# Optimization experiments

Measured on AMD Instinct MI355X. Metric: run time of the kernel, lower is better.

Reference implementation:

```python
import jax, jax.numpy as jnp
import numpy as np

B, P, ENC = 128, 196, 2048   # batch, num_pixels (14x14), encoder_dim
L, V = 50, 10000             # max caption length, vocab
A, D, E = 512, 512, 512      # attention_dim, decoder_dim, embed_dim


def setup_inputs() -> dict:
    key = jax.random.key(0)
    ks = jax.random.split(key, 24)
    def nrm(k, shape, s=0.02):
        return jax.random.normal(k, shape, jnp.float32) * s
    def uni(k, shape, lim=0.1):
        return jax.random.uniform(k, shape, jnp.float32, -lim, lim)
    cap_len = jax.random.randint(ks[2], (B,), 2, L + 1).at[0].set(L)  # ensure max dec_len = L-1 (static)
    return {
        "encoder_out": jax.random.normal(ks[0], (B, P, ENC), jnp.float32),
        "enc_cap": jax.random.randint(ks[1], (B, L), 0, V),
        "cap_len": cap_len,
        "emb_W": uni(ks[3], (V, E)),
        "init_h_W": nrm(ks[4], (D, ENC)), "init_h_b": jnp.zeros((D,), jnp.float32),
        "init_c_W": nrm(ks[5], (D, ENC)), "init_c_b": jnp.zeros((D,), jnp.float32),
        "enc_attn_W": nrm(ks[6], (A, ENC)), "enc_attn_b": jnp.zeros((A,), jnp.float32),
        "dec_attn_W": nrm(ks[7], (A, D)), "dec_attn_b": jnp.zeros((A,), jnp.float32),
        "full_attn_W": nrm(ks[8], (1, A)), "full_attn_b": jnp.zeros((1,), jnp.float32),
        "lstm_Wih": nrm(ks[9], (4 * D, E + ENC)), "lstm_Whh": nrm(ks[10], (4 * D, D)),
        "lstm_bih": jnp.zeros((4 * D,), jnp.float32), "lstm_bhh": jnp.zeros((4 * D,), jnp.float32),
        "fbeta_W": nrm(ks[11], (ENC, D)), "fbeta_b": jnp.zeros((ENC,), jnp.float32),
        "fc_W": uni(ks[12], (V, D)), "fc_b": jnp.zeros((V,), jnp.float32),
    }


def _forward(encoder_out, enc_cap, cap_len,
             emb_W, init_h_W, init_h_b, init_c_W, init_c_b,
             enc_attn_W, enc_attn_b, dec_attn_W, dec_attn_b,
             full_attn_W, full_attn_b, lstm_Wih, lstm_Whh, lstm_bih, lstm_bhh,
             fbeta_W, fbeta_b, fc_W, fc_b):
    Bsz, Pn, Ed = encoder_out.shape
    Dd = lstm_Whh.shape[1]
    # sort by decreasing length (stable, like torch.sort)
    sort_ind = jnp.argsort(-cap_len, stable=True)
    cap_sorted = cap_len[sort_ind]
    dec_len = cap_sorted - 1                       # [B]
    enc_s = encoder_out[sort_ind]                  # [B,P,ENC]
    caps_s = enc_cap[sort_ind]                     # [B,L]
    emb = emb_W[caps_s]                            # [B,L,E]
    enc_mean = enc_s.mean(axis=1)
    h0 = enc_mean @ init_h_W.T + init_h_b
    c0 = enc_mean @ init_c_W.T + init_c_b
    # precompute encoder attention features once (done per-step in torch, same values)
    enc_feat = jnp.einsum('bpe,ae->bpa', enc_s, enc_attn_W) + enc_attn_b  # [B,P,A]
    T = enc_cap.shape[1] - 1                       # static max decode steps

    def step(carry, t):
        h, c = carry
        active = (dec_len > t)[:, None].astype(h.dtype)         # [B,1]
        dec_feat = h @ dec_attn_W.T + dec_attn_b                # [B,A]
        attn = jax.nn.relu(enc_feat + dec_feat[:, None, :])     # [B,P,A]
        scores = attn @ full_attn_W[0] + full_attn_b[0]         # [B,P]
        alpha = jax.nn.softmax(scores, axis=1)                  # [B,P]
        ctx = jnp.einsum('bpe,bp->be', enc_s, alpha)            # [B,ENC]
        gate = jax.nn.sigmoid(h @ fbeta_W.T + fbeta_b)          # [B,ENC]
        ctx = gate * ctx
        x = jnp.concatenate([emb[:, t, :], ctx], axis=1)        # [B,E+ENC]
        gates = x @ lstm_Wih.T + lstm_bih + h @ lstm_Whh.T + lstm_bhh
        i_g, f_g, g_g, o_g = jnp.split(gates, 4, axis=1)
        c_new = jax.nn.sigmoid(f_g) * c + jax.nn.sigmoid(i_g) * jnp.tanh(g_g)
        h_new = jax.nn.sigmoid(o_g) * jnp.tanh(c_new)
        # dropout is identity in eval mode
        out = (h_new @ fc_W.T + fc_b) * active                  # zero rows past dec_len
        alpha = alpha * active
        # freeze state for finished sequences (matches torch's h[:bs] slicing)
        h = active * h_new + (1.0 - active) * h
        c = active * c_new + (1.0 - active) * c
        return (h, c), (out, alpha)

    (_, _), (outs, alphas) = jax.lax.scan(step, (h0, c0), jnp.arange(T))
    output = jnp.swapaxes(outs, 0, 1)    # [B,T,V]
    alphas = jnp.swapaxes(alphas, 0, 1)  # [B,T,P]
    return output, caps_s, dec_len, alphas, sort_ind


def reference(encoder_out, enc_cap, cap_len,
              emb_W, init_h_W, init_h_b, init_c_W, init_c_b,
              enc_attn_W, enc_attn_b, dec_attn_W, dec_attn_b,
              full_attn_W, full_attn_b, lstm_Wih, lstm_Whh, lstm_bih, lstm_bhh,
              fbeta_W, fbeta_b, fc_W, fc_b):
    return _forward(encoder_out, enc_cap, cap_len,
                    emb_W, init_h_W, init_h_b, init_c_W, init_c_b,
                    enc_attn_W, enc_attn_b, dec_attn_W, dec_attn_b,
                    full_attn_W, full_attn_b, lstm_Wih, lstm_Whh, lstm_bih, lstm_bhh,
                    fbeta_W, fbeta_b, fc_W, fc_b)
```

## Files before the change

### kernel.cpp

```cpp
#include <hip/hip_runtime.h>
#include <hip/hip_bf16.h>

#define B_    128
#define P_    196
#define ENCD  2048
#define LL    50
#define VV    10000
#define AA    512
#define DD    512
#define EE    512
#define TT    49
#define XKK   3072
#define PROJN 2560
#define VPAD  10048

#define OUT0_OFF 0
#define OUT1_OFF 62720000
#define OUT2_OFF 62726400
#define OUT3_OFF 62726528
#define OUT4_OFF 63955840

#define WS_SI      0ull
#define WS_DLEN    512ull
#define WS_BATTN   1024ull
#define WS_BLSTM   11264ull
#define WS_MEANS   19456ull
#define WS_H       1068032ull
#define WS_C       1330176ull
#define WS_HBF     1592320ull
#define WS_PROJ    1723392ull
#define WS_XCAT    6966272ull
#define WS_GATES   7752704ull
#define WS_HSTORE  16141312ull
#define WS_WPROJ   22563840ull
#define WS_WCAT    25185280ull
#define WS_FCW     37768192ull
#define WS_WENC    48057344ull
#define WS_EFEAT   50154496ull
#define WS_ENCBF   75844608ull
#define NEED_ENCBF 178605056ull

typedef __attribute__((ext_vector_type(4))) float f32x4;
typedef __attribute__((ext_vector_type(8))) short s16x8;

__device__ __forceinline__ float sigmoidf_(float x) { return 1.0f / (1.0f + __expf(-x)); }

__device__ __forceinline__ unsigned short f2bf(float x) {
    union { float f; unsigned int u; } v; v.f = x;
    unsigned int r = (v.u + 0x7FFFu + ((v.u >> 16) & 1u)) >> 16;
    return (unsigned short)r;
}
__device__ __forceinline__ float bf2f(unsigned short u) {
    return __uint_as_float(((unsigned int)u) << 16);
}

__device__ __forceinline__ void gload_lds16(const void* g, void* l) {
    __builtin_amdgcn_global_load_lds((const __attribute__((address_space(1))) void*)g,
                                     (__attribute__((address_space(3))) void*)l, 16, 0, 0);
}

__global__ void sort_kernel(const int* __restrict__ cap_len, const int* __restrict__ enc_cap,
                            int* __restrict__ si, int* __restrict__ dlen,
                            float* __restrict__ out_caps, float* __restrict__ out_dlen,
                            float* __restrict__ out_sind)
{
    __shared__ int cl[B_];
    __shared__ int rank_to_idx[B_];
    int i = threadIdx.x;
    cl[i] = cap_len[i];
    __syncthreads();
    int my = cl[i];
    int r = 0;
    for (int j = 0; j < B_; ++j) {
        int oj = cl[j];
        if (oj > my || (oj == my && j < i)) ++r;
    }
    rank_to_idx[r] = i;
    __syncthreads();
    int src = rank_to_idx[i];
    si[i] = src;
    int dl = cl[src] - 1;
    dlen[i] = dl;
    out_dlen[i] = (float)dl;
    out_sind[i] = (float)src;
    for (int k = 0; k < LL; ++k) out_caps[i * LL + k] = (float)enc_cap[src * LL + k];
}

__global__ void bias_cat_kernel(const float* __restrict__ dec_b, const float* __restrict__ fbeta_b,
                                const float* __restrict__ bih, const float* __restrict__ bhh,
                                float* __restrict__ b_attn, float* __restrict__ b_lstm)
{
    int i = blockIdx.x * 256 + threadIdx.x;
    if (i < AA) b_attn[i] = dec_b[i];
    else if (i < PROJN) b_attn[i] = fbeta_b[i - AA];
    if (i < 2048) b_lstm[i] = bih[i] + bhh[i];
}

__global__ void enc_mean_sorted(const float* __restrict__ enc, const int* __restrict__ si,
                                float* __restrict__ means)
{
    int idx = blockIdx.x * 256 + threadIdx.x;
    int b = idx >> 11, e = idx & 2047;
    const float* p = enc + (size_t)si[b] * P_ * ENCD + e;
    float s = 0.f;
    for (int q = 0; q < P_; ++q) s += p[(size_t)q * ENCD];
    means[idx] = s * (1.0f / 196.0f);
}

template<int MODE, bool CONV>
__launch_bounds__(256)
__global__ void mfma_gemm(const void* __restrict__ Av, const void* __restrict__ Wv,
                          const float* __restrict__ bias, const int* __restrict__ dlen,
                          float* __restrict__ Cf, unsigned short* __restrict__ Cbf,
                          int K, int KC, long long ldc, long long slabStride, int Nreal)
{
    __shared__ __align__(16) unsigned short As[2][128 * 32];
    __shared__ __align__(16) unsigned short Ws[2][64 * 32];
    const int tid  = threadIdx.x;
    const int wave = tid >> 6, lane = tid & 63;
    const int m0 = (MODE == 2 ? blockIdx.x : blockIdx.y) * 128;
    const int n0 = (MODE == 2 ? blockIdx.y : blockIdx.x) * 64;
    const int z  = blockIdx.z;
    const int kbeg = z * KC;
    const int nt = KC / 32;
    const int r16 = lane & 15, kg = lane >> 4;

    f32x4 acc[8];
    #pragma unroll
    for (int i = 0; i < 8; ++i) acc[i] = f32x4{0.f, 0.f, 0.f, 0.f};

    const int a_off0 = wave * 2048 + lane * 16;
    const int a_row0 = a_off0 >> 6, a_c0 = (a_off0 >> 4) & 3;
    const int a_off1 = a_off0 + 1024;
    const int a_row1 = a_off1 >> 6, a_c1 = (a_off1 >> 4) & 3;
    const int w_off  = wave * 1024 + lane * 16;
    const int w_row  = w_off >> 6,  w_c  = (w_off >> 4) & 3;
    const int c_arow = tid >> 1, c_acb = (tid & 1) * 16;
    const int c_wrow = tid >> 2, c_wcb = (tid & 3) * 8;

    int buf = 0;

    if constexpr (!CONV) {
        const unsigned short* A = (const unsigned short*)Av;
        const unsigned short* W = (const unsigned short*)Wv;
        gload_lds16(A + (size_t)(m0 + a_row0) * K + kbeg + a_c0 * 8, &As[0][wave * 1024]);
        gload_lds16(A + (size_t)(m0 + a_row1) * K + kbeg + a_c1 * 8, &As[0][wave * 1024 + 512]);
        gload_lds16(W + (size_t)(n0 + w_row)  * K + kbeg + w_c  * 8, &Ws[0][wave * 512]);
        __syncthreads();
        for (int it = 0; it < nt; ++it) {
            if (it + 1 < nt) {
                int k1 = kbeg + (it + 1) * 32;
                gload_lds16(A + (size_t)(m0 + a_row0) * K + k1 + a_c0 * 8, &As[buf ^ 1][wave * 1024]);
                gload_lds16(A + (size_t)(m0 + a_row1) * K + k1 + a_c1 * 8, &As[buf ^ 1][wave * 1024 + 512]);
                gload_lds16(W + (size_t)(n0 + w_row)  * K + k1 + w_c  * 8, &Ws[buf ^ 1][wave * 512]);
            }
            s16x8 bfrag = *(const s16x8*)&Ws[buf][(wave * 16 + r16) * 32 + kg * 8];
            #pragma unroll
            for (int i = 0; i < 8; ++i) {
                s16x8 afrag = *(const s16x8*)&As[buf][(i * 16 + r16) * 32 + kg * 8];
                acc[i] = __builtin_amdgcn_mfma_f32_16x16x32_bf16(afrag, bfrag, acc[i], 0, 0, 0);
            }
            __syncthreads();
            buf ^= 1;
        }
    } else {
        const float* A = (const float*)Av;
        const float* W = (const float*)Wv;
        float ra[16], rw[8];
        #pragma unroll
        for (int j = 0; j < 16; ++j) ra[j] = A[(size_t)(m0 + c_arow) * K + kbeg + c_acb + j];
        #pragma unroll
        for (int j = 0; j < 8; ++j)  rw[j] = W[(size_t)(n0 + c_wrow) * K + kbeg + c_wcb + j];
        {
            unsigned short t0[16], t1[8];
            #pragma unroll
            for (int j = 0; j < 16; ++j) t0[j] = f2bf(ra[j]);
            #pragma unroll
            for (int j = 0; j < 8; ++j)  t1[j] = f2bf(rw[j]);
            *(s16x8*)&As[0][c_arow * 32 + c_acb]     = *(s16x8*)&t0[0];
            *(s16x8*)&As[0][c_arow * 32 + c_acb + 8] = *(s16x8*)&t0[8];
            *(s16x8*)&Ws[0][c_wrow * 32 + c_wcb]     = *(s16x8*)&t1[0];
        }
        __syncthreads();
        for (int it = 0; it < nt; ++it) {
            float ra2[16], rw2[8];
            bool more = (it + 1 < nt);
            if (more) {
                int k1 = kbeg + (it + 1) * 32;
                #pragma unroll
                for (int j = 0; j < 16; ++j) ra2[j] = A[(size_t)(m0 + c_arow) * K + k1 + c_acb + j];
                #pragma unroll
                for (int j = 0; j < 8; ++j)  rw2[j] = W[(size_t)(n0 + c_wrow) * K + k1 + c_wcb + j];
            }
            s16x8 bfrag = *(const s16x8*)&Ws[buf][(wave * 16 + r16) * 32 + kg * 8];
            #pragma unroll
            for (int i = 0; i < 8; ++i) {
                s16x8 afrag = *(const s16x8*)&As[buf][(i * 16 + r16) * 32 + kg * 8];
                acc[i] = __builtin_amdgcn_mfma_f32_16x16x32_bf16(afrag, bfrag, acc[i], 0, 0, 0);
            }
            if (more) {
                unsigned short t0[16], t1[8];
                #pragma unroll
                for (int j = 0; j < 16; ++j) t0[j] = f2bf(ra2[j]);
                #pragma unroll
                for (int j = 0; j < 8; ++j)  t1[j] = f2bf(rw2[j]);
                *(s16x8*)&As[buf ^ 1][c_arow * 32 + c_acb]     = *(s16x8*)&t0[0];
                *(s16x8*)&As[buf ^ 1][c_arow * 32 + c_acb + 8] = *(s16x8*)&t0[8];
                *(s16x8*)&Ws[buf ^ 1][c_wrow * 32 + c_wcb]     = *(s16x8*)&t1[0];
            }
            __syncthreads();
            buf ^= 1;
        }
    }

    int n = n0 + wave * 16 + r16;
    float bv = 0.f;
    if (bias && z == 0) bv = (MODE == 2) ? (n < Nreal ? bias[n] : 0.f) : bias[n];
    float* Cz = Cf + (size_t)z * slabStride;
    #pragma unroll
    for (int i = 0; i < 8; ++i) {
        #pragma unroll
        for (int r = 0; r < 4; ++r) {
            int m = m0 + i * 16 + kg * 4 + r;
            float v = acc[i][r] + bv;
            if (MODE == 0) {
                Cz[(size_t)m * ldc + n] = v;
            } else if (MODE == 1) {
                Cbf[(size_t)m * ldc + n] = f2bf(v);
            } else {
                int bb = m & 127, tt2 = m >> 7;
                if (n < Nreal)
                    Cf[((size_t)bb * TT + tt2) * VV + n] = (dlen[bb] > tt2) ? v : 0.f;
            }
        }
    }
}

template<int NS>
__global__ void scores_raw_kernel(const unsigned short* __restrict__ efeat,
                                  const float* __restrict__ proj, const float* __restrict__ battn,
                                  const float* __restrict__ full_W, const float* __restrict__ full_b,
                                  const int* __restrict__ si, const int* __restrict__ dlen,
                                  float* __restrict__ sc_out, int t)
{
    int b = blockIdx.x, q = blockIdx.y;
    if (dlen[b] <= t) return;
    int tid = threadIdx.x, wave = tid >> 6, lane = tid & 63;
    __shared__ float df[AA];
    __shared__ float wf[AA];
    const size_t ps = (size_t)B_ * PROJN;
    const float* pz = proj + (size_t)b * PROJN;
    for (int i = tid; i < AA; i += 256) {
        float v = battn[i];
        #pragma unroll
        for (int z = 0; z < NS; ++z) v += pz[z * ps + i];
        df[i] = v; wf[i] = full_W[i];
    }
    __syncthreads();
    int sb = si[b];
    const float fb = full_b[0];
    float dfv[8], wfv[8];
    #pragma unroll
    for (int j = 0; j < 8; ++j) { dfv[j] = df[lane * 8 + j]; wfv[j] = wf[lane * 8 + j]; }
    int pbeg = q * 49;
    for (int p = pbeg + wave; p < pbeg + 49; p += 4) {
        const unsigned short* ef = efeat + ((size_t)sb * P_ + p) * AA + lane * 8;
        s16x8 ev = *(const s16x8*)ef;
        float s = 0.f;
        #pragma unroll
        for (int j = 0; j < 8; ++j) {
            float v = bf2f((unsigned short)ev[j]) + dfv[j];
            v = v > 0.f ? v : 0.f;
            s += v * wfv[j];
        }
        #pragma unroll
        for (int off = 32; off; off >>= 1) s += __shfl_down(s, off);
        if (lane == 0) sc_out[b * P_ + p] = s + fb;
    }
}

template<int NS>
__global__ void ctx_fused_kernel(const float* __restrict__ sc_in,
                                 const float* __restrict__ proj, const float* __restrict__ battn,
                                 const int* __restrict__ si, const int* __restrict__ dlen,
                                 const int* __restrict__ enc_cap, const float* __restrict__ emb_W,
                                 const unsigned short* __restrict__ h_bf,
                                 const unsigned short* __restrict__ encbf,
                                 const float* __restrict__ encf, int use_bf,
                                 float* __restrict__ alphas_out, unsigned short* __restrict__ xcat, int t)
{
    int b = blockIdx.y, x = blockIdx.x, tid = threadIdx.x;
    int wave = tid >> 6, lane = tid & 63;
    bool active = dlen[b] > t;
    if (!active) {
        if (x == 0 && tid < P_) alphas_out[((size_t)b * TT + t) * P_ + tid] = 0.f;
        return;
    }
    __shared__ float al[P_];
    __shared__ float red[8];
    float v = (tid < P_) ? sc_in[b * P_ + tid] : -1e30f;
    float m = v;
    #pragma unroll
    for (int off = 32; off; off >>= 1) m = fmaxf(m, __shfl_down(m, off));
    if (lane == 0) red[wave] = m;
    __syncthreads();
    if (tid == 0) red[4] = fmaxf(fmaxf(red[0], red[1]), fmaxf(red[2], red[3]));
    __syncthreads();
    m = red[4];
    float e = (tid < P_) ? __expf(v - m) : 0.f;
    float s = e;
    #pragma unroll
    for (int off = 32; off; off >>= 1) s += __shfl_down(s, off);
    if (lane == 0) red[wave] = s;
    __syncthreads();
    if (tid == 0) red[5] = 1.0f / (red[0] + red[1] + red[2] + red[3]);
    __syncthreads();
    float inv = red[5];
    if (tid < P_) al[tid] = e * inv;
    __syncthreads();

    int sb = si[b];
    if (x == 0) {
        if (tid < P_) alphas_out[((size_t)b * TT + t) * P_ + tid] = al[tid];
        int tok = enc_cap[sb * LL + t];
        for (int k = tid; k < EE; k += 256) {
            xcat[(size_t)b * XKK + k]        = f2bf(emb_W[(size_t)tok * EE + k]);
            xcat[(size_t)b * XKK + 2560 + k] = h_bf[b * DD + k];
        }
    }

    int e0 = x * 1024 + tid * 4;
    float a0 = 0.f, a1 = 0.f, a2 = 0.f, a3 = 0.f;
    if (use_bf) {
        const unsigned short* base = encbf + (size_t)sb * P_ * ENCD + e0;
        #pragma unroll 7
        for (int p = 0; p < P_; ++p) {
            uint2 u = *(const uint2*)(base + (size_t)p * ENCD);
            float alp = al[p];
            a0 = fmaf(alp, __uint_as_float(u.x << 16), a0);
            a1 = fmaf(alp, __uint_as_float(u.x & 0xffff0000u), a1);
            a2 = fmaf(alp, __uint_as_float(u.y << 16), a2);
            a3 = fmaf(alp, __uint_as_float(u.y & 0xffff0000u), a3);
        }
    } else {
        const float* base = encf + (size_t)sb * P_ * ENCD + e0;
        #pragma unroll 7
        for (int p = 0; p < P_; ++p) {
            float4 u = *(const float4*)(base + (size_t)p * ENCD);
            float alp = al[p];
            a0 = fmaf(alp, u.x, a0); a1 = fmaf(alp, u.y, a1);
            a2 = fmaf(alp, u.z, a2); a3 = fmaf(alp, u.w, a3);
        }
    }
    const float* pz = proj + (size_t)b * PROJN;
    const size_t ps = (size_t)B_ * PROJN;
    int ei = AA + e0;
    float4 gl = *(const float4*)&battn[ei];
    #pragma unroll
    for (int z = 0; z < NS; ++z) {
        float4 gp = *(const float4*)&pz[z * ps + ei];
        gl.x += gp.x; gl.y += gp.y; gl.z += gp.z; gl.w += gp.w;
    }
    ushort4 xo;
    xo.x = f2bf(a0 * sigmoidf_(gl.x));
    xo.y = f2bf(a1 * sigmoidf_(gl.y));
    xo.z = f2bf(a2 * sigmoidf_(gl.z));
    xo.w = f2bf(a3 * sigmoidf_(gl.w));
    *(ushort4*)&xcat[(size_t)b * XKK + EE + e0] = xo;
}

template<int NS>
__global__ void pointwise_kernel(const float* __restrict__ gates, const float* __restrict__ blstm,
                                 const int* __restrict__ dlen,
                                 float* __restrict__ h, float* __restrict__ c,
                                 unsigned short* __restrict__ h_bf, unsigned short* __restrict__ hstore,
                                 int t)
{
    int idx = blockIdx.x * 256 + threadIdx.x;
    int b = idx >> 9, d = idx & 511;
    bool act = dlen[b] > (t - 1);
    if (!act) {
        hstore[((size_t)(t - 1) * B_ + b) * DD + d] = 0;
        return;
    }
    const size_t slab = (size_t)B_ * 2048;
    const float* g = gates + (size_t)b * 2048;
    float gi = blstm[d], gf = blstm[512 + d], gg = blstm[1024 + d], go = blstm[1536 + d];
    #pragma unroll
    for (int z = 0; z < NS; ++z) {
        gi += g[z * slab + d];
        gf += g[z * slab + 512 + d];
        gg += g[z * slab + 1024 + d];
        go += g[z * slab + 1536 + d];
    }
    float cn = sigmoidf_(gf) * c[idx] + sigmoidf_(gi) * tanhf(gg);
    float hn = sigmoidf_(go) * tanhf(cn);
    unsigned short hb = f2bf(hn);
    hstore[((size_t)(t - 1) * B_ + b) * DD + d] = hb;
    h[idx] = hn; c[idx] = cn;
    h_bf[idx] = hb;
}

__global__ void conv_bf16_kernel(const float* __restrict__ src, unsigned short* __restrict__ dst, int n4)
{
    for (int i = blockIdx.x * 256 + threadIdx.x; i < n4; i += gridDim.x * 256) {
        float4 v = ((const float4*)src)[i];
        ushort4 o;
        o.x = f2bf(v.x); o.y = f2bf(v.y); o.z = f2bf(v.z); o.w = f2bf(v.w);
        ((ushort4*)dst)[i] = o;
    }
}
__global__ void conv_wproj_kernel(const float* __restrict__ dec_W, const float* __restrict__ fbeta_W,
                                  unsigned short* __restrict__ dst)
{
    int k = blockIdx.x * 256 + threadIdx.x, n = blockIdx.y;
    float v = (n < AA) ? dec_W[(size_t)n * DD + k] : fbeta_W[(size_t)(n - AA) * DD + k];
    dst[(size_t)n * DD + k] = f2bf(v);
}
__global__ void conv_wcat_kernel(const float* __restrict__ Wih, const float* __restrict__ Whh,
                                 unsigned short* __restrict__ dst)
{
    int k = blockIdx.x * 256 + threadIdx.x, n = blockIdx.y;
    float v = (k < 2560) ? Wih[(size_t)n * 2560 + k] : Whh[(size_t)n * DD + (k - 2560)];
    dst[(size_t)n * XKK + k] = f2bf(v);
}
__global__ void conv_fcw_kernel(const float* __restrict__ fc_W, unsigned short* __restrict__ dst)
{
    int k = blockIdx.x * 256 + threadIdx.x, n = blockIdx.y;
    float v = (n < VV) ? fc_W[(size_t)n * DD + k] : 0.f;
    dst[(size_t)n * DD + k] = f2bf(v);
}

extern "C" void kernel_launch(void* const* d_in, const int* in_sizes, int n_in,
                              void* d_out, int out_size, void* d_ws, size_t ws_size,
                              hipStream_t stream)
{
    const float* encoder_out = (const float*)d_in[0];
    const int*   enc_cap     = (const int*)d_in[1];
    const int*   cap_len     = (const int*)d_in[2];
    const float* emb_W       = (const float*)d_in[3];
    const float* init_h_W    = (const float*)d_in[4];
    const float* init_h_b    = (const float*)d_in[5];
    const float* init_c_W    = (const float*)d_in[6];
    const float* init_c_b    = (const float*)d_in[7];
    const float* enc_attn_W  = (const float*)d_in[8];
    const float* enc_attn_b  = (const float*)d_in[9];
    const float* dec_attn_W  = (const float*)d_in[10];
    const float* dec_attn_b  = (const float*)d_in[11];
    const float* full_attn_W = (const float*)d_in[12];
    const float* full_attn_b = (const float*)d_in[13];
    const float* lstm_Wih    = (const float*)d_in[14];
    const float* lstm_Whh    = (const float*)d_in[15];
    const float* lstm_bih    = (const float*)d_in[16];
    const float* lstm_bhh    = (const float*)d_in[17];
    const float* fbeta_W     = (const float*)d_in[18];
    const float* fbeta_b     = (const float*)d_in[19];
    const float* fc_W        = (const float*)d_in[20];
    const float* fc_b        = (const float*)d_in[21];

    char* wsb = (char*)d_ws;
    int*   si     = (int*)(wsb + WS_SI);
    int*   dlen   = (int*)(wsb + WS_DLEN);
    float* battn  = (float*)(wsb + WS_BATTN);
    float* blstm  = (float*)(wsb + WS_BLSTM);
    float* means  = (float*)(wsb + WS_MEANS);
    float* sc     = (float*)(wsb + WS_MEANS + 4096);
    float* h      = (float*)(wsb + WS_H);
    float* c      = (float*)(wsb + WS_C);
    unsigned short* h_bf   = (unsigned short*)(wsb + WS_HBF);
    float* proj   = (float*)(wsb + WS_PROJ);
    unsigned short* xcat   = (unsigned short*)(wsb + WS_XCAT);
    float* gates  = (float*)(wsb + WS_GATES);
    unsigned short* hstore = (unsigned short*)(wsb + WS_HSTORE);
    unsigned short* wproj  = (unsigned short*)(wsb + WS_WPROJ);
    unsigned short* wcat   = (unsigned short*)(wsb + WS_WCAT);
    unsigned short* fcw    = (unsigned short*)(wsb + WS_FCW);
    unsigned short* wenc   = (unsigned short*)(wsb + WS_WENC);
    unsigned short* efeat  = (unsigned short*)(wsb + WS_EFEAT);
    unsigned short* encbf  = (unsigned short*)(wsb + WS_ENCBF);

    float* out      = (float*)d_out;
    float* out0     = out + OUT0_OFF;
    float* out_caps = out + OUT1_OFF;
    float* out_dlen = out + OUT2_OFF;
    float* alphas   = out + OUT3_OFF;
    float* out_sind = out + OUT4_OFF;

    const int use_encbf = (ws_size >= NEED_ENCBF) ? 1 : 0;

    sort_kernel<<<1, B_, 0, stream>>>(cap_len, enc_cap, si, dlen, out_caps, out_dlen, out_sind);
    bias_cat_kernel<<<10, 256, 0, stream>>>(dec_attn_b, fbeta_b, lstm_bih, lstm_bhh, battn, blstm);
    enc_mean_sorted<<<(B_ * ENCD) / 256, 256, 0, stream>>>(encoder_out, si, means);

    mfma_gemm<0, true><<<dim3(DD / 64, 1, 1), 256, 0, stream>>>(
        means, init_h_W, init_h_b, nullptr, h, nullptr, ENCD, ENCD, DD, 0, DD);
    mfma_gemm<0, true><<<dim3(DD / 64, 1, 1), 256, 0, stream>>>(
        means, init_c_W, init_c_b, nullptr, c, nullptr, ENCD, ENCD, DD, 0, DD);
    conv_bf16_kernel<<<64, 256, 0, stream>>>(h, h_bf, (B_ * DD) / 4);

    conv_wproj_kernel<<<dim3(2, PROJN), 256, 0, stream>>>(dec_attn_W, fbeta_W, wproj);
    conv_wcat_kernel<<<dim3(12, 2048), 256, 0, stream>>>(lstm_Wih, lstm_Whh, wcat);
    conv_fcw_kernel<<<dim3(2, VPAD), 256, 0, stream>>>(fc_W, fcw);
    conv_bf16_kernel<<<256, 256, 0, stream>>>(enc_attn_W, wenc, (AA * ENCD) / 4);
    if (use_encbf)
        conv_bf16_kernel<<<2048, 256, 0, stream>>>(encoder_out, encbf, (B_ * P_ * ENCD) / 4);

    if (use_encbf)
        mfma_gemm<1, false><<<dim3(AA / 64, (B_ * P_) / 128, 1), 256, 0, stream>>>(
            encbf, wenc, enc_attn_b, nullptr, nullptr, efeat, ENCD, ENCD, AA, 0, AA);
    else
        mfma_gemm<1, true><<<dim3(AA / 64, (B_ * P_) / 128, 1), 256, 0, stream>>>(
            encoder_out, enc_attn_W, enc_attn_b, nullptr, nullptr, efeat, ENCD, ENCD, AA, 0, AA);

    for (int t = 0; t < TT; ++t) {
        if (t > 0)
            pointwise_kernel<8><<<(B_ * DD) / 256, 256, 0, stream>>>(
                gates, blstm, dlen, h, c, h_bf, hstore, t);

        mfma_gemm<0, false><<<dim3(PROJN / 64, 1, 4), 256, 0, stream>>>(
            h_bf, wproj, nullptr, nullptr, proj, nullptr, DD, 128, PROJN, (long long)B_ * PROJN, PROJN);

        scores_raw_kernel<4><<<dim3(B_, 4), 256, 0, stream>>>(
            efeat, proj, battn, full_attn_W, full_attn_b, si, dlen, sc, t);

        ctx_fused_kernel<4><<<dim3(2, B_), 256, 0, stream>>>(
            sc, proj, battn, si, dlen, enc_cap, emb_W, h_bf,
            encbf, encoder_out, use_encbf, alphas, xcat, t);

        mfma_gemm<0, false><<<dim3(2048 / 64, 1, 8), 256, 0, stream>>>(
            xcat, wcat, nullptr, nullptr, gates, nullptr, XKK, 384, 2048, (long long)B_ * 2048, 2048);
    }
    pointwise_kernel<8><<<(B_ * DD) / 256, 256, 0, stream>>>(
        gates, blstm, dlen, h, c, h_bf, hstore, TT);

    mfma_gemm<2, false><<<dim3(TT, VPAD / 64, 1), 256, 0, stream>>>(
        hstore, fcw, fc_b, dlen, out0, nullptr, DD, DD, VV, 0, VV);
}
```

Before: 2.970 ms.

## Fuse attention scoring into context kernel and widen GEMM K-tile to 64

Merges the separate attention-score kernel into the context/softmax kernel, so each block computes all 196 pixel scores itself with one thread per pixel. This removes one launch per timestep and the scores round-trip through global memory. In exchange, the score work is duplicated across the two x-blocks per batch row, and each thread now runs a 512-long serial dot product. It also adds a K-tile template parameter to the bf16 MFMA GEMM and uses 64 for the non-converting GEMMs, halving the loop iterations and barriers at the cost of double the LDS per block.

Result: no change. 2.973 ms (+0.1%).

```diff
diff --git a/kernel.cpp b/kernel.cpp
--- a/kernel.cpp
+++ b/kernel.cpp
@@ -107,34 +107,31 @@
     means[idx] = s * (1.0f / 196.0f);
 }
 
-template<int MODE, bool CONV>
+template<int MODE, bool CONV, int BK2>
 __launch_bounds__(256)
 __global__ void mfma_gemm(const void* __restrict__ Av, const void* __restrict__ Wv,
                           const float* __restrict__ bias, const int* __restrict__ dlen,
                           float* __restrict__ Cf, unsigned short* __restrict__ Cbf,
                           int K, int KC, long long ldc, long long slabStride, int Nreal)
 {
-    __shared__ __align__(16) unsigned short As[2][128 * 32];
-    __shared__ __align__(16) unsigned short Ws[2][64 * 32];
+    constexpr int RB = BK2 * 2;
+    constexpr int AL = (128 * RB) / 4096;
+    constexpr int WL = (64 * RB) / 4096;
+    __shared__ __align__(16) unsigned short As[2][128 * BK2];
+    __shared__ __align__(16) unsigned short Ws[2][64 * BK2];
     const int tid  = threadIdx.x;
     const int wave = tid >> 6, lane = tid & 63;
     const int m0 = (MODE == 2 ? blockIdx.x : blockIdx.y) * 128;
     const int n0 = (MODE == 2 ? blockIdx.y : blockIdx.x) * 64;
     const int z  = blockIdx.z;
     const int kbeg = z * KC;
-    const int nt = KC / 32;
+    const int nt = KC / BK2;
     const int r16 = lane & 15, kg = lane >> 4;
 
     f32x4 acc[8];
     #pragma unroll
     for (int i = 0; i < 8; ++i) acc[i] = f32x4{0.f, 0.f, 0.f, 0.f};
 
-    const int a_off0 = wave * 2048 + lane * 16;
-    const int a_row0 = a_off0 >> 6, a_c0 = (a_off0 >> 4) & 3;
-    const int a_off1 = a_off0 + 1024;
-    const int a_row1 = a_off1 >> 6, a_c1 = (a_off1 >> 4) & 3;
-    const int w_off  = wave * 1024 + lane * 16;
-    const int w_row  = w_off >> 6,  w_c  = (w_off >> 4) & 3;
     const int c_arow = tid >> 1, c_acb = (tid & 1) * 16;
     const int c_wrow = tid >> 2, c_wcb = (tid & 3) * 8;
 
@@ -143,27 +140,49 @@
     if constexpr (!CONV) {
         const unsigned short* A = (const unsigned short*)Av;
         const unsigned short* W = (const unsigned short*)Wv;
-        gload_lds16(A + (size_t)(m0 + a_row0) * K + kbeg + a_c0 * 8, &As[0][wave * 1024]);
-        gload_lds16(A + (size_t)(m0 + a_row1) * K + kbeg + a_c1 * 8, &As[0][wave * 1024 + 512]);
-        gload_lds16(W + (size_t)(n0 + w_row)  * K + kbeg + w_c  * 8, &Ws[0][wave * 512]);
+        #pragma unroll
+        for (int s = 0; s < AL; ++s) {
+            int L = s * 4096 + wave * 1024 + lane * 16;
+            gload_lds16(A + (size_t)(m0 + L / RB) * K + kbeg + (L % RB) / 2,
+                        &As[0][(s * 4096 + wave * 1024) / 2]);
+        }
+        #pragma unroll
+        for (int s = 0; s < WL; ++s) {
+            int L = s * 4096 + wave * 1024 + lane * 16;
+            gload_lds16(W + (size_t)(n0 + L / RB) * K + kbeg + (L % RB) / 2,
+                        &Ws[0][(s * 4096 + wave * 1024) / 2]);
+        }
         __syncthreads();
         for (int it = 0; it < nt; ++it) {
             if (it + 1 < nt) {
-                int k1 = kbeg + (it + 1) * 32;
-                gload_lds16(A + (size_t)(m0 + a_row0) * K + k1 + a_c0 * 8, &As[buf ^ 1][wave * 1024]);
-                gload_lds16(A + (size_t)(m0 + a_row1) * K + k1 + a_c1 * 8, &As[buf ^ 1][wave * 1024 + 512]);
-                gload_lds16(W + (size_t)(n0 + w_row)  * K + k1 + w_c  * 8, &Ws[buf ^ 1][wave * 512]);
-            }
-            s16x8 bfrag = *(const s16x8*)&Ws[buf][(wave * 16 + r16) * 32 + kg * 8];
+                int k1 = kbeg + (it + 1) * BK2;
+                #pragma unroll
+                for (int s = 0; s < AL; ++s) {
+                    int L = s * 4096 + wave * 1024 + lane * 16;
+                    gload_lds16(A + (size_t)(m0 + L / RB) * K + k1 + (L % RB) / 2,
+                                &As[buf ^ 1][(s * 4096 + wave * 1024) / 2]);
+                }
+                #pragma unroll
+                for (int s = 0; s < WL; ++s) {
+                    int L = s * 4096 + wave * 1024 + lane * 16;
+                    gload_lds16(W + (size_t)(n0 + L / RB) * K + k1 + (L % RB) / 2,
+                                &Ws[buf ^ 1][(s * 4096 + wave * 1024) / 2]);
+                }
+            }
             #pragma unroll
-            for (int i = 0; i < 8; ++i) {
-                s16x8 afrag = *(const s16x8*)&As[buf][(i * 16 + r16) * 32 + kg * 8];
-                acc[i] = __builtin_amdgcn_mfma_f32_16x16x32_bf16(afrag, bfrag, acc[i], 0, 0, 0);
+            for (int kk2 = 0; kk2 < BK2 / 32; ++kk2) {
+                s16x8 bfrag = *(const s16x8*)&Ws[buf][(wave * 16 + r16) * BK2 + kk2 * 32 + kg * 8];
+                #pragma unroll
+                for (int i = 0; i < 8; ++i) {
+                    s16x8 afrag = *(const s16x8*)&As[buf][(i * 16 + r16) * BK2 + kk2 * 32 + kg * 8];
+                    acc[i] = __builtin_amdgcn_mfma_f32_16x16x32_bf16(afrag, bfrag, acc[i], 0, 0, 0);
+                }
             }
             __syncthreads();
             buf ^= 1;
         }
     } else {
+        static_assert(!CONV || BK2 == 32, "CONV path requires BK2==32");
         const float* A = (const float*)Av;
         const float* W = (const float*)Wv;
         float ra[16], rw[8];
@@ -237,57 +256,15 @@
 }
 
 template<int NS>
-__global__ void scores_raw_kernel(const unsigned short* __restrict__ efeat,
-                                  const float* __restrict__ proj, const float* __restrict__ battn,
-                                  const float* __restrict__ full_W, const float* __restrict__ full_b,
-                                  const int* __restrict__ si, const int* __restrict__ dlen,
-                                  float* __restrict__ sc_out, int t)
-{
-    int b = blockIdx.x, q = blockIdx.y;
-    if (dlen[b] <= t) return;
-    int tid = threadIdx.x, wave = tid >> 6, lane = tid & 63;
-    __shared__ float df[AA];
-    __shared__ float wf[AA];
-    const size_t ps = (size_t)B_ * PROJN;
-    const float* pz = proj + (size_t)b * PROJN;
-    for (int i = tid; i < AA; i += 256) {
-        float v = battn[i];
-        #pragma unroll
-        for (int z = 0; z < NS; ++z) v += pz[z * ps + i];
-        df[i] = v; wf[i] = full_W[i];
-    }
-    __syncthreads();
-    int sb = si[b];
-    const float fb = full_b[0];
-    float dfv[8], wfv[8];
-    #pragma unroll
-    for (int j = 0; j < 8; ++j) { dfv[j] = df[lane * 8 + j]; wfv[j] = wf[lane * 8 + j]; }
-    int pbeg = q * 49;
-    for (int p = pbeg + wave; p < pbeg + 49; p += 4) {
-        const unsigned short* ef = efeat + ((size_t)sb * P_ + p) * AA + lane * 8;
-        s16x8 ev = *(const s16x8*)ef;
-        float s = 0.f;
-        #pragma unroll
-        for (int j = 0; j < 8; ++j) {
-            float v = bf2f((unsigned short)ev[j]) + dfv[j];
-            v = v > 0.f ? v : 0.f;
-            s += v * wfv[j];
-        }
-        #pragma unroll
-        for (int off = 32; off; off >>= 1) s += __shfl_down(s, off);
-        if (lane == 0) sc_out[b * P_ + p] = s + fb;
-    }
-}
-
-template<int NS>
-__global__ void ctx_fused_kernel(const float* __restrict__ sc_in,
-                                 const float* __restrict__ proj, const float* __restrict__ battn,
-                                 const int* __restrict__ si, const int* __restrict__ dlen,
-                                 const int* __restrict__ enc_cap, const float* __restrict__ emb_W,
-                                 const unsigned short* __restrict__ h_bf,
-                                 const unsigned short* __restrict__ encbf,
-                                 const float* __restrict__ encf, int use_bf,
-                                 float* __restrict__ alphas_out, unsigned short* __restrict__ xcat, int t)
+__global__ void attn_kernel(const unsigned short* __restrict__ efeat,
+                            const float* __restrict__ proj, const float* __restrict__ battn,
+                            const float* __restrict__ full_W, const float* __restrict__ full_b,
+                            const int* __restrict__ si, const int* __restrict__ dlen,
+                            const int* __restrict__ enc_cap, const float* __restrict__ emb_W,
+                            const unsigned short* __restrict__ h_bf,
+                            const unsigned short* __restrict__ encbf,
+                            const float* __restrict__ encf, int use_bf,
+                            float* __restrict__ alphas_out, unsigned short* __restrict__ xcat, int t)
 {
     int b = blockIdx.y, x = blockIdx.x, tid = threadIdx.x;
     int wave = tid >> 6, lane = tid & 63;
@@ -296,9 +273,35 @@
         if (x == 0 && tid < P_) alphas_out[((size_t)b * TT + t) * P_ + tid] = 0.f;
         return;
     }
-    __shared__ float al[P_];
+    __shared__ float df[AA];
+    __shared__ float wf[AA];
+    __shared__ float sal[P_];
     __shared__ float red[8];
-    float v = (tid < P_) ? sc_in[b * P_ + tid] : -1e30f;
+    const float* pz = proj + (size_t)b * PROJN;
+    const size_t ps = (size_t)B_ * PROJN;
+    for (int i = tid; i < AA; i += 256) {
+        float v = battn[i];
+        #pragma unroll
+        for (int z = 0; z < NS; ++z) v += pz[z * ps + i];
+        df[i] = v; wf[i] = full_W[i];
+    }
+    __syncthreads();
+    int sb = si[b];
+    float s = full_b[0];
+    if (tid < P_) {
+        const unsigned short* ef = efeat + ((size_t)sb * P_ + tid) * AA;
+        #pragma unroll 8
+        for (int e8 = 0; e8 < 64; ++e8) {
+            s16x8 ev = *(const s16x8*)(ef + e8 * 8);
+            #pragma unroll
+            for (int j = 0; j < 8; ++j) {
+                float v = bf2f((unsigned short)ev[j]) + df[e8 * 8 + j];
+                v = v > 0.f ? v : 0.f;
+                s = fmaf(v, wf[e8 * 8 + j], s);
+            }
+        }
+    }
+    float v = (tid < P_) ? s : -1e30f;
     float m = v;
     #pragma unroll
     for (int off = 32; off; off >>= 1) m = fmaxf(m, __shfl_down(m, off));
@@ -308,26 +311,24 @@
     __syncthreads();
     m = red[4];
     float e = (tid < P_) ? __expf(v - m) : 0.f;
-    float s = e;
+    float ssum = e;
     #pragma unroll
-    for (int off = 32; off; off >>= 1) s += __shfl_down(s, off);
-    if (lane == 0) red[wave] = s;
+    for (int off = 32; off; off >>= 1) ssum += __shfl_down(ssum, off);
+    if (lane == 0) red[wave] = ssum;
     __syncthreads();
     if (tid == 0) red[5] = 1.0f / (red[0] + red[1] + red[2] + red[3]);
     __syncthreads();
-    float inv = red[5];
-    if (tid < P_) al[tid] = e * inv;
-    __syncthreads();
-
-    int sb = si[b];
+    float al = e * red[5];
+    if (tid < P_) sal[tid] = al;
     if (x == 0) {
-        if (tid < P_) alphas_out[((size_t)b * TT + t) * P_ + tid] = al[tid];
+        if (tid < P_) alphas_out[((size_t)b * TT + t) * P_ + tid] = al;
         int tok = enc_cap[sb * LL + t];
         for (int k = tid; k < EE; k += 256) {
             xcat[(size_t)b * XKK + k]        = f2bf(emb_W[(size_t)tok * EE + k]);
             xcat[(size_t)b * XKK + 2560 + k] = h_bf[b * DD + k];
         }
     }
+    __syncthreads();
 
     int e0 = x * 1024 + tid * 4;
     float a0 = 0.f, a1 = 0.f, a2 = 0.f, a3 = 0.f;
@@ -336,7 +337,7 @@
         #pragma unroll 7
         for (int p = 0; p < P_; ++p) {
             uint2 u = *(const uint2*)(base + (size_t)p * ENCD);
-            float alp = al[p];
+            float alp = sal[p];
             a0 = fmaf(alp, __uint_as_float(u.x << 16), a0);
             a1 = fmaf(alp, __uint_as_float(u.x & 0xffff0000u), a1);
             a2 = fmaf(alp, __uint_as_float(u.y << 16), a2);
@@ -347,13 +348,11 @@
         #pragma unroll 7
         for (int p = 0; p < P_; ++p) {
             float4 u = *(const float4*)(base + (size_t)p * ENCD);
-            float alp = al[p];
+            float alp = sal[p];
             a0 = fmaf(alp, u.x, a0); a1 = fmaf(alp, u.y, a1);
             a2 = fmaf(alp, u.z, a2); a3 = fmaf(alp, u.w, a3);
         }
     }
-    const float* pz = proj + (size_t)b * PROJN;
-    const size_t ps = (size_t)B_ * PROJN;
     int ei = AA + e0;
     float4 gl = *(const float4*)&battn[ei];
     #pragma unroll
@@ -464,7 +463,6 @@
     float* battn  = (float*)(wsb + WS_BATTN);
     float* blstm  = (float*)(wsb + WS_BLSTM);
     float* means  = (float*)(wsb + WS_MEANS);
-    float* sc     = (float*)(wsb + WS_MEANS + 4096);
     float* h      = (float*)(wsb + WS_H);
     float* c      = (float*)(wsb + WS_C);
     unsigned short* h_bf   = (unsigned short*)(wsb + WS_HBF);
@@ -492,9 +490,9 @@
     bias_cat_kernel<<<10, 256, 0, stream>>>(dec_attn_b, fbeta_b, lstm_bih, lstm_bhh, battn, blstm);
     enc_mean_sorted<<<(B_ * ENCD) / 256, 256, 0, stream>>>(encoder_out, si, means);
 
-    mfma_gemm<0, true><<<dim3(DD / 64, 1, 1), 256, 0, stream>>>(
+    mfma_gemm<0, true, 32><<<dim3(DD / 64, 1, 1), 256, 0, stream>>>(
         means, init_h_W, init_h_b, nullptr, h, nullptr, ENCD, ENCD, DD, 0, DD);
-    mfma_gemm<0, true><<<dim3(DD / 64, 1, 1), 256, 0, stream>>>(
+    mfma_gemm<0, true, 32><<<dim3(DD / 64, 1, 1), 256, 0, stream>>>(
         means, init_c_W, init_c_b, nullptr, c, nullptr, ENCD, ENCD, DD, 0, DD);
     conv_bf16_kernel<<<64, 256, 0, stream>>>(h, h_bf, (B_ * DD) / 4);
 
@@ -506,10 +504,10 @@
         conv_bf16_kernel<<<2048, 256, 0, stream>>>(encoder_out, encbf, (B_ * P_ * ENCD) / 4);
 
     if (use_encbf)
-        mfma_gemm<1, false><<<dim3(AA / 64, (B_ * P_) / 128, 1), 256, 0, stream>>>(
+        mfma_gemm<1, false, 64><<<dim3(AA / 64, (B_ * P_) / 128, 1), 256, 0, stream>>>(
             encbf, wenc, enc_attn_b, nullptr, nullptr, efeat, ENCD, ENCD, AA, 0, AA);
     else
-        mfma_gemm<1, true><<<dim3(AA / 64, (B_ * P_) / 128, 1), 256, 0, stream>>>(
+        mfma_gemm<1, true, 32><<<dim3(AA / 64, (B_ * P_) / 128, 1), 256, 0, stream>>>(
             encoder_out, enc_attn_W, enc_attn_b, nullptr, nullptr, efeat, ENCD, ENCD, AA, 0, AA);
 
     for (int t = 0; t < TT; ++t) {
@@ -517,22 +515,19 @@
             pointwise_kernel<8><<<(B_ * DD) / 256, 256, 0, stream>>>(
                 gates, blstm, dlen, h, c, h_bf, hstore, t);
 
-        mfma_gemm<0, false><<<dim3(PROJN / 64, 1, 4), 256, 0, stream>>>(
+        mfma_gemm<0, false, 64><<<dim3(PROJN / 64, 1, 4), 256, 0, stream>>>(
             h_bf, wproj, nullptr, nullptr, proj, nullptr, DD, 128, PROJN, (long long)B_ * PROJN, PROJN);
 
-        scores_raw_kernel<4><<<dim3(B_, 4), 256, 0, stream>>>(
-            efeat, proj, battn, full_attn_W, full_attn_b, si, dlen, sc, t);
-
-        ctx_fused_kernel<4><<<dim3(2, B_), 256, 0, stream>>>(
-            sc, proj, battn, si, dlen, enc_cap, emb_W, h_bf,
+        attn_kernel<4><<<dim3(2, B_), 256, 0, stream>>>(
+            efeat, proj, battn, full_attn_W, full_attn_b, si, dlen, enc_cap, emb_W, h_bf,
             encbf, encoder_out, use_encbf, alphas, xcat, t);
 
-        mfma_gemm<0, false><<<dim3(2048 / 64, 1, 8), 256, 0, stream>>>(
+        mfma_gemm<0, false, 64><<<dim3(2048 / 64, 1, 8), 256, 0, stream>>>(
             xcat, wcat, nullptr, nullptr, gates, nullptr, XKK, 384, 2048, (long long)B_ * 2048, 2048);
     }
     pointwise_kernel<8><<<(B_ * DD) / 256, 256, 0, stream>>>(
         gates, blstm, dlen, h, c, h_bf, hstore, TT);
 
-    mfma_gemm<2, false><<<dim3(TT, VPAD / 64, 1), 256, 0, stream>>>(
+    mfma_gemm<2, false, 64><<<dim3(TT, VPAD / 64, 1), 256, 0, stream>>>(
         hstore, fcw, fc_b, dlen, out0, nullptr, DD, DD, VV, 0, VV);
 }
```
